# Kernel tuning notes

Measured on AMD Instinct MI355X. Metric: run time of the kernel, lower is better.

The kernel has to match this reference:

```python
import jax, jax.numpy as jnp
import numpy as np

N, E, G = 100000, 3200000, 5000
EPS = 1e-5
HEADS, HC = 8, 16


def setup_inputs() -> dict:
    key = jax.random.key(0)
    k = jax.random.split(key, 12)

    def lin(kk, fi, fo):
        return (jax.random.normal(kk, (fi, fo), jnp.float32) / np.sqrt(fi)).astype(jnp.float32)

    return {
        "x": jax.random.normal(k[0], (N, 20), jnp.float32),
        "edge_index": jax.random.randint(k[1], (2, E), 0, N, dtype=jnp.int32),
        "batch": jnp.sort(jax.random.randint(k[2], (N,), 0, G, dtype=jnp.int32)),
        "W1": lin(k[3], 20, 64), "b1": jnp.zeros((64,), jnp.float32),
        "g1": jnp.ones((64,), jnp.float32), "be1": jnp.zeros((64,), jnp.float32),
        "W2": lin(k[4], 64, 32), "b2": jnp.zeros((32,), jnp.float32),
        "g2": jnp.ones((32,), jnp.float32), "be2": jnp.zeros((32,), jnp.float32),
        "W3": lin(k[5], 32, 16), "b3": jnp.zeros((16,), jnp.float32),
        "g3": jnp.ones((16,), jnp.float32), "be3": jnp.zeros((16,), jnp.float32),
        "Wg": lin(k[6], 16, HEADS * HC),
        "att_src": jax.random.normal(k[7], (HEADS, HC), jnp.float32) * 0.1,
        "att_dst": jax.random.normal(k[8], (HEADS, HC), jnp.float32) * 0.1,
        "bg": jnp.zeros((HC,), jnp.float32),
        "Wf": lin(k[9], 16, 3), "bf": jnp.zeros((3,), jnp.float32),
    }


def reference(x, edge_index, batch,
              W1, b1, g1, be1, W2, b2, g2, be2, W3, b3, g3, be3,
              Wg, att_src, att_dst, bg, Wf, bf):
    src, dst = edge_index[0], edge_index[1]
    loop = jnp.arange(N, dtype=src.dtype)
    src_sl = jnp.concatenate([src, loop])  # self-loops (GCN + GAT add_self_loops)
    dst_sl = jnp.concatenate([dst, loop])

    # GCN symmetric normalization D^-1/2 (A+I) D^-1/2
    deg = jax.ops.segment_sum(jnp.ones_like(src_sl, dtype=jnp.float32), dst_sl, N)
    dinv = jnp.where(deg > 0, 1.0 / jnp.sqrt(deg), 0.0)
    norm = (dinv[src_sl] * dinv[dst_sl])[:, None]  # [E+N, 1]

    def gcn(h, W, b):
        h = h @ W
        return jax.ops.segment_sum(h[src_sl] * norm, dst_sl, N) + b

    def bn_relu(h, g, b):  # BatchNorm1d (train-mode batch stats) + ReLU
        mu = h.mean(0)
        var = ((h - mu) ** 2).mean(0)
        return jax.nn.relu(g * (h - mu) * jax.lax.rsqrt(var + EPS) + b)

    h = bn_relu(gcn(x, W1, b1), g1, be1)   # dropout = identity (eval)
    h = bn_relu(gcn(h, W2, b2), g2, be2)
    h = bn_relu(gcn(h, W3, b3), g3, be3)

    # GATConv: heads=8, concat=False (mean over heads), eval -> no dropout
    xg = (h @ Wg).reshape(N, HEADS, HC)
    a_src = (xg * att_src).sum(-1)  # [N, H]
    a_dst = (xg * att_dst).sum(-1)
    logit = jax.nn.leaky_relu(a_src[src_sl] + a_dst[dst_sl], 0.2)  # [E+N, H]
    m = jax.ops.segment_max(logit, dst_sl, N)          # segment softmax over dst
    e = jnp.exp(logit - m[dst_sl])
    s = jax.ops.segment_sum(e, dst_sl, N)
    alpha = e / s[dst_sl]
    agg = jax.ops.segment_sum(xg[src_sl] * alpha[:, :, None], dst_sl, N)  # [N,H,C]
    hg = agg.mean(1) + bg  # [N, 16]

    pooled = jax.ops.segment_sum(hg, batch, G)  # global_add_pool -> [G, 16]
    return pooled @ Wf + bf  # [G, 3]
```

## Files before the change

### kernel.cpp

```cpp
#include <hip/hip_runtime.h>
#include <hip/hip_fp16.h>

constexpr int NN = 100000;
constexpr int EE = 3200000;
constexpr int GG = 5000;
constexpr float BNEPS = 1e-5f;

constexpr int BINS = 128;
constexpr int NPB = (NN + BINS - 1) / BINS;
constexpr int BCHUNK = 8192;
constexpr int NBCH = (EE + BCHUNK - 1) / BCHUNK;
constexpr int BINCAP2 = 96;
constexpr int BINREG = 27648;
constexpr int LCAP = 26624;
constexpr int CTR_STRIDE = 32;

typedef int int4v __attribute__((ext_vector_type(4)));


__global__ __launch_bounds__(1024) void bin_edges(const int* __restrict__ ei,
                                                  uint2* __restrict__ pairs,
                                                  int* __restrict__ binCur) {
    __shared__ int bcnt[BINS];
    __shared__ int bbase[BINS];
    __shared__ uint2 buf[BINS][BINCAP2];
    const int t = threadIdx.x;
    const int lane = t & 63, wv = t >> 6;
    for (int ch = blockIdx.x; ch < NBCH; ch += gridDim.x) {
        for (int k = t; k < BINS; k += 1024) bcnt[k] = 0;
        __syncthreads();
        const int qbase = ch * (BCHUNK / 4);
#pragma unroll
        for (int rep = 0; rep < 2; ++rep) {
            const int q = qbase + rep * 1024 + t;
            if (q < EE / 4) {
                int4v d = __builtin_nontemporal_load((const int4v*)(ei + EE) + q);
                int4v s = __builtin_nontemporal_load((const int4v*)ei + q);
                int dd[4] = {d.x, d.y, d.z, d.w};
                int ss[4] = {s.x, s.y, s.z, s.w};
#pragma unroll
                for (int k = 0; k < 4; ++k) {
                    int o = dd[k] / NPB;
                    int p = atomicAdd(&bcnt[o], 1);
                    if (p < BINCAP2) {
                        buf[o][p] = make_uint2((unsigned)dd[k], (unsigned)ss[k]);
                    } else {
                        int gp = atomicAdd(&binCur[o * CTR_STRIDE], 1);
                        pairs[(size_t)o * BINREG + gp] =
                            make_uint2((unsigned)dd[k], (unsigned)ss[k]);
                    }
                }
            }
        }
        __syncthreads();
        if (t < BINS) {
            int c = bcnt[t] < BINCAP2 ? bcnt[t] : BINCAP2;
            bbase[t] = atomicAdd(&binCur[t * CTR_STRIDE], c);
            bcnt[t] = c;
        }
        __syncthreads();
        for (int o = wv; o < BINS; o += 16) {
            const int c = bcnt[o];
            const size_t base = (size_t)o * BINREG + bbase[o];
            for (int k = lane; k < c; k += 64) pairs[base + k] = buf[o][k];
        }
        __syncthreads();
    }
}


__global__ void bin_base(const int* __restrict__ binCur, int* __restrict__ binBase) {
    __shared__ int s[BINS];
    const int t = threadIdx.x;
    const int v = binCur[t * CTR_STRIDE];
    s[t] = v;
    __syncthreads();
    for (int off = 1; off < BINS; off <<= 1) {
        int add = (t >= off) ? s[t - off] : 0;
        __syncthreads();
        s[t] += add;
        __syncthreads();
    }
    binBase[t] = s[t] - v;
}


__global__ __launch_bounds__(1024) void scatter_lds(const uint2* __restrict__ pairs,
                                                    const int* __restrict__ binCur,
                                                    const int* __restrict__ binBase,
                                                    int* __restrict__ rowptr,
                                                    float* __restrict__ dinv,
                                                    int* __restrict__ colA) {
    __shared__ int scnt[NPB];
    __shared__ int sscan[1024];
    __shared__ int lbuf[LCAP];
    const int b = blockIdx.x;
    const int t = threadIdx.x;
    const int lo = b * NPB;
    const int hi = (lo + NPB < NN) ? lo + NPB : NN;
    const int nb = hi - lo;
    const int tot = binCur[b * CTR_STRIDE];
    const int base = binBase[b];
    const uint2* p = pairs + (size_t)b * BINREG;
    for (int k = t; k < nb; k += 1024) scnt[k] = 0;
    __syncthreads();
    for (int q = t; q < tot; q += 1024) atomicAdd(&scnt[p[q].x - lo], 1);
    __syncthreads();
    const int myc = (t < nb) ? scnt[t] : 0;
    sscan[t] = myc;
    __syncthreads();
    for (int off = 1; off < 1024; off <<= 1) {
        int add = (t >= off) ? sscan[t - off] : 0;
        __syncthreads();
        sscan[t] += add;
        __syncthreads();
    }
    const int excl = sscan[t] - myc;
    if (t < nb) {
        rowptr[lo + t] = base + excl;
        dinv[lo + t] = rsqrtf((float)(myc + 1));
        scnt[t] = excl;
    }
    if (b == BINS - 1 && t == 0) rowptr[NN] = base + tot;
    __syncthreads();
    for (int q = t; q < tot; q += 1024) {
        uint2 e = p[q];
        int pos = atomicAdd(&scnt[e.x - lo], 1);
        if (pos < LCAP) lbuf[pos] = (int)e.y;
        else colA[base + pos] = (int)e.y;
    }
    __syncthreads();
    const int m = tot < LCAP ? tot : LCAP;
    for (int k = t; k < m; k += 1024) colA[base + k] = lbuf[k];
}


__global__ void scale_x(const float* __restrict__ x, const float* __restrict__ dinv,
                        __half* __restrict__ xsc) {
    int idx = blockIdx.x * blockDim.x + threadIdx.x;
    if (idx < NN * 20) {
        int n = idx / 20;
        xsc[idx] = __float2half(x[idx] * dinv[n]);
    }
}


template <int FIN, int FOUT, bool AFFINE, bool SCALED, bool STATS>
__global__ void gemm_k(const float* __restrict__ hin,
                       const float* __restrict__ sumsIn, const float* __restrict__ ssqIn,
                       const float* __restrict__ g, const float* __restrict__ be,
                       const float* __restrict__ W, const float* __restrict__ dinv,
                       const float* __restrict__ bias,
                       float* __restrict__ outF, __half* __restrict__ outH,
                       float* __restrict__ sumsOut, float* __restrict__ ssqOut) {
    constexpr int NB = 256 / FOUT;
    __shared__ float Wl[FIN * FOUT];
    __shared__ float rows[NB][FIN];
    __shared__ float aa[AFFINE ? FIN : 1], bb[AFFINE ? FIN : 1];
    const int t = threadIdx.x;
    if constexpr (AFFINE) {
        if (t < FIN) {
            float mu = sumsIn[t] / (float)NN;
            float var = ssqIn[t] / (float)NN - mu * mu;
            float a = g[t] * rsqrtf(var + BNEPS);
            aa[t] = a;
            bb[t] = be[t] - mu * a;
        }
    }
    for (int i = t; i < FIN * FOUT; i += 256) Wl[i] = W[i];
    const int c = t % FOUT, s = t / FOUT;
    const int ngrp = (NN + NB - 1) / NB;
    float sAcc = 0.f, qAcc = 0.f;
    for (int grp = blockIdx.x; grp < ngrp; grp += gridDim.x) {
        __syncthreads();
        for (int i = t; i < NB * FIN; i += 256) {
            int sn = i / FIN, k = i % FIN;
            int n2 = grp * NB + sn;
            float v = 0.f;
            if (n2 < NN) {
                v = hin[(size_t)n2 * FIN + k];
                if constexpr (AFFINE) {
                    v = aa[k] * v + bb[k];
                    v = v > 0.f ? v : 0.f;
                }
            }
            rows[sn][k] = v;
        }
        __syncthreads();
        int node = grp * NB + s;
        if (node < NN) {
            float acc = 0.f;
#pragma unroll
            for (int k = 0; k < FIN; ++k) acc += rows[s][k] * Wl[k * FOUT + c];
            if constexpr (SCALED) {
                outH[(size_t)node * FOUT + c] = __float2half(acc * dinv[node]);
            } else {
                float val = acc + bias[c];
                outF[(size_t)node * FOUT + c] = val;
                if constexpr (STATS) { sAcc += val; qAcc += val * val; }
            }
        }
    }
    if constexpr (STATS) {
        __shared__ float ls[FOUT], lq[FOUT];
        __syncthreads();
        if (t < FOUT) { ls[t] = 0.f; lq[t] = 0.f; }
        __syncthreads();
        atomicAdd(&ls[c], sAcc);
        atomicAdd(&lq[c], qAcc);
        __syncthreads();
        if (t < FOUT) { atomicAdd(&sumsOut[t], ls[t]); atomicAdd(&ssqOut[t], lq[t]); }
    }
}


template <int H2, int OUTF, bool STATS>
__global__ void agg_half(const __half2* __restrict__ src, const int* __restrict__ rowptr,
                         const int* __restrict__ colA, const float* __restrict__ dinv,
                         const float* __restrict__ bias, float* __restrict__ out,
                         float* __restrict__ sumsOut, float* __restrict__ ssqOut) {
    constexpr int SUB = 64 / H2;
    const int lane = threadIdx.x & 63;
    const int wid = (blockIdx.x * blockDim.x + threadIdx.x) >> 6;
    const int totalWaves = (gridDim.x * blockDim.x) >> 6;
    const int f = lane % H2;
    const int sub = lane / H2;
    const int stride = totalWaves * SUB;
    float bx = 0.f, by = 0.f;
    if (bias != nullptr) {
        bx = bias[2 * f];
        by = (2 * f + 1 < OUTF) ? bias[2 * f + 1] : 0.f;
    }
    const int i0 = (sub < SUB) ? wid * SUB + sub : NN;
    float sx = 0.f, qx = 0.f, sy = 0.f, qy = 0.f;
    for (int i = i0; i < NN; i += stride) {
        const int r0 = rowptr[i], r1 = rowptr[i + 1];
        float2 acc = __half22float2(src[(size_t)i * H2 + f]);
        float2 acc2 = {0.f, 0.f};
        int e = r0;
        for (; e + 3 < r1; e += 4) {
            int j0 = colA[e], j1 = colA[e + 1], j2 = colA[e + 2], j3 = colA[e + 3];
            float2 v0 = __half22float2(src[(size_t)j0 * H2 + f]);
            float2 v1 = __half22float2(src[(size_t)j1 * H2 + f]);
            float2 v2 = __half22float2(src[(size_t)j2 * H2 + f]);
            float2 v3 = __half22float2(src[(size_t)j3 * H2 + f]);
            acc.x += v0.x + v1.x;
            acc.y += v0.y + v1.y;
            acc2.x += v2.x + v3.x;
            acc2.y += v2.y + v3.y;
        }
        for (; e < r1; ++e) {
            float2 v = __half22float2(src[(size_t)colA[e] * H2 + f]);
            acc.x += v.x; acc.y += v.y;
        }
        acc.x += acc2.x; acc.y += acc2.y;
        const float d = dinv[i];
        float vx = d * acc.x + bx;
        out[(size_t)i * OUTF + 2 * f] = vx;
        if constexpr (STATS) { sx += vx; qx += vx * vx; }
        if (2 * f + 1 < OUTF) {
            float vy = d * acc.y + by;
            out[(size_t)i * OUTF + 2 * f + 1] = vy;
            if constexpr (STATS) { sy += vy; qy += vy * vy; }
        }
    }
    if constexpr (STATS) {
        __shared__ float ls[OUTF], lq[OUTF];
        const int t = threadIdx.x;
        if (t < OUTF) { ls[t] = 0.f; lq[t] = 0.f; }
        __syncthreads();
        atomicAdd(&ls[2 * f], sx);
        atomicAdd(&lq[2 * f], qx);
        if (2 * f + 1 < OUTF) {
            atomicAdd(&ls[2 * f + 1], sy);
            atomicAdd(&lq[2 * f + 1], qy);
        }
        __syncthreads();
        if (t < OUTF) { atomicAdd(&sumsOut[t], ls[t]); atomicAdd(&ssqOut[t], lq[t]); }
    }
}


__global__ void gat_mats(const float* __restrict__ Wg, const float* __restrict__ att_src,
                         const float* __restrict__ att_dst, const float* __restrict__ Wf,
                         const float* __restrict__ bg, float* __restrict__ Psrc,
                         float* __restrict__ Pdst, float* __restrict__ M,
                         float* __restrict__ bgW) {
    int t = threadIdx.x;
    if (t < 128) {
        int k = t >> 3, h = t & 7;
        float s = 0.f, d = 0.f;
        for (int c = 0; c < 16; ++c) {
            float wv = Wg[k * 128 + h * 16 + c];
            s += wv * att_src[h * 16 + c];
            d += wv * att_dst[h * 16 + c];
        }
        Psrc[k * 8 + h] = s;
        Pdst[k * 8 + h] = d;
    } else if (t < 512) {
        int m = t - 128;
        if (m < 384) {
            int hk = m / 3, j = m - hk * 3;
            int H = hk >> 4, k = hk & 15;
            float s = 0.f;
            for (int c = 0; c < 16; ++c) s += Wg[k * 128 + H * 16 + c] * Wf[c * 3 + j];
            M[hk * 3 + j] = 0.125f * s;
        }
    } else if (t < 515) {
        int j = t - 512;
        float s = 0.f;
        for (int c = 0; c < 16; ++c) s += bg[c] * Wf[c * 3 + j];
        bgW[j] = s;
    }
}


__global__ void gat_pre2(const float* __restrict__ h3,
                         const float* __restrict__ sums3, const float* __restrict__ ssq3,
                         const float* __restrict__ g3, const float* __restrict__ be3,
                         const float* __restrict__ Psrc, const float* __restrict__ Pdst,
                         __half* __restrict__ z, float* __restrict__ asrc,
                         float* __restrict__ adst) {
    __shared__ float Ps[128], Pd[128], aa[16], bb[16];
    int t = threadIdx.x;
    if (t < 128) { Ps[t] = Psrc[t]; Pd[t] = Pdst[t]; }
    if (t < 16) {
        float mu = sums3[t] / (float)NN;
        float var = ssq3[t] / (float)NN - mu * mu;
        float a = g3[t] * rsqrtf(var + BNEPS);
        aa[t] = a;
        bb[t] = be3[t] - mu * a;
    }
    __syncthreads();
    int n = blockIdx.x * blockDim.x + t;
    if (n >= NN) return;
    float zv[16];
#pragma unroll
    for (int k = 0; k < 16; ++k) {
        float v = h3[(size_t)n * 16 + k];
        v = aa[k] * v + bb[k];
        zv[k] = v > 0.f ? v : 0.f;
    }
    __half2 zh[8];
#pragma unroll
    for (int k = 0; k < 8; ++k) zh[k] = __floats2half2_rn(zv[2 * k], zv[2 * k + 1]);
    float4* zo = (float4*)(z + (size_t)n * 16);
    zo[0] = ((float4*)zh)[0];
    zo[1] = ((float4*)zh)[1];
    float as[8], ad[8];
#pragma unroll
    for (int h = 0; h < 8; ++h) { as[h] = 0.f; ad[h] = 0.f; }
#pragma unroll
    for (int k = 0; k < 16; ++k) {
        float zk = zv[k];
#pragma unroll
        for (int h = 0; h < 8; ++h) {
            as[h] += zk * Ps[k * 8 + h];
            ad[h] += zk * Pd[k * 8 + h];
        }
    }
    float4* a4 = (float4*)(asrc + (size_t)n * 8);
    a4[0] = make_float4(as[0], as[1], as[2], as[3]);
    a4[1] = make_float4(as[4], as[5], as[6], as[7]);
    float4* d4 = (float4*)(adst + (size_t)n * 8);
    d4[0] = make_float4(ad[0], ad[1], ad[2], ad[3]);
    d4[1] = make_float4(ad[4], ad[5], ad[6], ad[7]);
}


__device__ __forceinline__ float leaky02(float x) { return x > 0.f ? x : 0.2f * x; }

__global__ void gat_agg5(const float2* __restrict__ z2, const float* __restrict__ asrc,
                         const float* __restrict__ adst, const int* __restrict__ rowptr,
                         const int* __restrict__ colA, __half* __restrict__ Sn) {
    const int lane = threadIdx.x & 63;
    const int q = lane & 3;
    const int hh = (lane >> 2) & 1;
    const int sub = lane >> 3;
    const int wid = (blockIdx.x * blockDim.x + threadIdx.x) >> 6;
    const int totalWaves = (gridDim.x * blockDim.x) >> 6;
    const float4* asrc4 = (const float4*)asrc;
    const float4* adst4 = (const float4*)adst;
    for (int i = wid; i < NN; i += totalWaves) {
        const int r0 = rowptr[i], r1 = rowptr[i + 1];
        const float4 adh = adst4[(size_t)i * 2 + hh];
        float acc[4][4];
        float wsum[4];
        {
            float4 a = asrc4[(size_t)i * 2 + hh];
            float2 zr = z2[(size_t)i * 4 + q];
            const __half2* zp = (const __half2*)&zr;
            float2 f0 = __half22float2(zp[0]), f1 = __half22float2(zp[1]);
            float zf[4] = {f0.x, f0.y, f1.x, f1.y};
            float wq[4];
            wq[0] = (sub == 0) ? __expf(leaky02(a.x + adh.x)) : 0.f;
            wq[1] = (sub == 0) ? __expf(leaky02(a.y + adh.y)) : 0.f;
            wq[2] = (sub == 0) ? __expf(leaky02(a.z + adh.z)) : 0.f;
            wq[3] = (sub == 0) ? __expf(leaky02(a.w + adh.w)) : 0.f;
#pragma unroll
            for (int h = 0; h < 4; ++h) {
                wsum[h] = wq[h];
#pragma unroll
                for (int k = 0; k < 4; ++k) acc[h][k] = wq[h] * zf[k];
            }
        }
        for (int e = r0; e < r1; e += 8) {
            const int ee = e + sub;
            const bool val = ee < r1;
            const int j = val ? colA[ee] : i;
            float4 a = asrc4[(size_t)j * 2 + hh];
            float2 zr = z2[(size_t)j * 4 + q];
            const __half2* zp = (const __half2*)&zr;
            float2 f0 = __half22float2(zp[0]), f1 = __half22float2(zp[1]);
            float zf[4] = {f0.x, f0.y, f1.x, f1.y};
            float wq[4];
            wq[0] = val ? __expf(leaky02(a.x + adh.x)) : 0.f;
            wq[1] = val ? __expf(leaky02(a.y + adh.y)) : 0.f;
            wq[2] = val ? __expf(leaky02(a.z + adh.z)) : 0.f;
            wq[3] = val ? __expf(leaky02(a.w + adh.w)) : 0.f;
#pragma unroll
            for (int h = 0; h < 4; ++h) {
                wsum[h] += wq[h];
#pragma unroll
                for (int k = 0; k < 4; ++k) acc[h][k] += wq[h] * zf[k];
            }
        }
#pragma unroll
        for (int off = 8; off < 64; off <<= 1) {
#pragma unroll
            for (int h = 0; h < 4; ++h) {
                wsum[h] += __shfl_xor(wsum[h], off);
#pragma unroll
                for (int k = 0; k < 4; ++k) acc[h][k] += __shfl_xor(acc[h][k], off);
            }
        }
        if (lane < 8) {
#pragma unroll
            for (int h = 0; h < 4; ++h) {
                const float inv = 1.f / wsum[h];
                __half2 o[2];
                o[0] = __floats2half2_rn(acc[h][0] * inv, acc[h][1] * inv);
                o[1] = __floats2half2_rn(acc[h][2] * inv, acc[h][3] * inv);
                *(float2*)(Sn + (size_t)i * 128 + (hh * 4 + h) * 16 + q * 4) = *(float2*)o;
            }
        }
    }
}


__global__ void graph_bounds(const int* __restrict__ batch, int* __restrict__ gstart) {
    int n = blockIdx.x * blockDim.x + threadIdx.x;
    if (n < NN) {
        int bn = batch[n];
        int bp = (n == 0) ? -1 : batch[n - 1];
        for (int g = bp + 1; g <= bn; ++g) gstart[g] = n;
        if (n == NN - 1)
            for (int g = bn + 1; g <= GG; ++g) gstart[g] = NN;
    }
}


__global__ void pool_final(const __half2* __restrict__ Sn2, const int* __restrict__ gstart,
                           const float* __restrict__ M, const float* __restrict__ bgW,
                           const float* __restrict__ bf, float* __restrict__ out) {
    const int lane = threadIdx.x & 63;
    const int g = (blockIdx.x * blockDim.x + threadIdx.x) >> 6;
    if (g >= GG) return;
    const int n0 = gstart[g], n1 = gstart[g + 1];
    float2 s = {0.f, 0.f};
    for (int n = n0; n < n1; ++n) {
        float2 v = __half22float2(Sn2[(size_t)n * 64 + lane]);
        s.x += v.x;
        s.y += v.y;
    }
    float o[3];
#pragma unroll
    for (int j = 0; j < 3; ++j)
        o[j] = s.x * M[(2 * lane) * 3 + j] + s.y * M[(2 * lane + 1) * 3 + j];
#pragma unroll
    for (int off = 1; off < 64; off <<= 1) {
#pragma unroll
        for (int j = 0; j < 3; ++j) o[j] += __shfl_xor(o[j], off);
    }
    if (lane == 0) {
        float cnt = (float)(n1 - n0);
#pragma unroll
        for (int j = 0; j < 3; ++j) out[g * 3 + j] = o[j] + cnt * bgW[j] + bf[j];
    }
}


extern "C" void kernel_launch(void* const* d_in, const int* in_sizes, int n_in,
                              void* d_out, int out_size, void* d_ws, size_t ws_size,
                              hipStream_t stream) {
    const float* x = (const float*)d_in[0];
    const int* ei = (const int*)d_in[1];
    const int* batch = (const int*)d_in[2];
    const float* W1 = (const float*)d_in[3];  const float* b1 = (const float*)d_in[4];
    const float* g1 = (const float*)d_in[5];  const float* be1 = (const float*)d_in[6];
    const float* W2 = (const float*)d_in[7];  const float* b2 = (const float*)d_in[8];
    const float* g2 = (const float*)d_in[9];  const float* be2 = (const float*)d_in[10];
    const float* W3 = (const float*)d_in[11]; const float* b3 = (const float*)d_in[12];
    const float* g3 = (const float*)d_in[13]; const float* be3 = (const float*)d_in[14];
    const float* Wg = (const float*)d_in[15];
    const float* att_src = (const float*)d_in[16];
    const float* att_dst = (const float*)d_in[17];
    const float* bg = (const float*)d_in[18];
    const float* Wf = (const float*)d_in[19];
    const float* bf = (const float*)d_in[20];
    float* out = (float*)d_out;

    char* w = (char*)d_ws;
    auto alloc = [&](size_t bytes) -> char* {
        char* p = w;
        w += (bytes + 255) & ~(size_t)255;
        return p;
    };
    int* binCur = (int*)alloc((size_t)BINS * CTR_STRIDE * 4);
    float* sums1 = (float*)alloc(64 * 4); float* ssq1 = (float*)alloc(64 * 4);
    float* sums2 = (float*)alloc(32 * 4); float* ssq2 = (float*)alloc(32 * 4);
    float* sums3 = (float*)alloc(16 * 4); float* ssq3 = (float*)alloc(16 * 4);
    size_t zeroBytes = (size_t)(w - (char*)d_ws);
    int* binBase = (int*)alloc((size_t)BINS * 4);
    float* Psrc = (float*)alloc(128 * 4);
    float* Pdst = (float*)alloc(128 * 4);
    float* Mm = (float*)alloc(384 * 4);
    float* bgW = (float*)alloc(3 * 4);
    int* gstart = (int*)alloc((size_t)(GG + 1) * 4);
    int* rowptr = (int*)alloc((size_t)(NN + 1) * 4);
    int* colA = (int*)alloc((size_t)EE * 4);
    float* dinv = (float*)alloc((size_t)NN * 4);
    char* A = alloc((size_t)NN * 64 * 4);
    char* B = alloc((size_t)NN * 64 * 4);

    uint2*  pairs = (uint2*)A;
    __half* xsc  = (__half*)B;
    float*  aggx = (float*)(B + (size_t)NN * 32 * 2);
    float*  h1   = (float*)A;
    __half* hs2  = (__half*)B;
    float*  h2   = (float*)(B + (size_t)NN * 32 * 2);
    __half* hs3  = (__half*)A;
    float*  h3   = (float*)(A + (size_t)NN * 16 * 2);
    __half* z    = (__half*)(A + (size_t)NN * 24 * 4);
    float*  asrc = (float*)(A + (size_t)NN * 32 * 4);
    float*  adst = (float*)(A + (size_t)NN * 40 * 4);
    __half* Sn   = (__half*)B;

    hipMemsetAsync(d_ws, 0, zeroBytes, stream);

    bin_edges<<<256, 1024, 0, stream>>>(ei, pairs, binCur);
    bin_base<<<1, BINS, 0, stream>>>(binCur, binBase);
    scatter_lds<<<BINS, 1024, 0, stream>>>(pairs, binCur, binBase, rowptr, dinv, colA);
    gat_mats<<<1, 1024, 0, stream>>>(Wg, att_src, att_dst, Wf, bg, Psrc, Pdst, Mm, bgW);
    graph_bounds<<<(NN + 255) / 256, 256, 0, stream>>>(batch, gstart);

    scale_x<<<(NN * 20 + 255) / 256, 256, 0, stream>>>(x, dinv, xsc);
    agg_half<10, 20, false><<<2048, 256, 0, stream>>>((const __half2*)xsc, rowptr, colA, dinv,
                                                      nullptr, aggx, nullptr, nullptr);
    gemm_k<20, 64, false, false, true><<<2048, 256, 0, stream>>>(
        aggx, nullptr, nullptr, nullptr, nullptr, W1, dinv, b1, h1, nullptr, sums1, ssq1);

    gemm_k<64, 32, true, true, false><<<2048, 256, 0, stream>>>(
        h1, sums1, ssq1, g1, be1, W2, dinv, nullptr, nullptr, hs2, nullptr, nullptr);
    agg_half<16, 32, true><<<2048, 256, 0, stream>>>((const __half2*)hs2, rowptr, colA, dinv,
                                                     b2, h2, sums2, ssq2);

    gemm_k<32, 16, true, true, false><<<2048, 256, 0, stream>>>(
        h2, sums2, ssq2, g2, be2, W3, dinv, nullptr, nullptr, hs3, nullptr, nullptr);
    agg_half<8, 16, true><<<2048, 256, 0, stream>>>((const __half2*)hs3, rowptr, colA, dinv,
                                                    b3, h3, sums3, ssq3);

    gat_pre2<<<(NN + 255) / 256, 256, 0, stream>>>(h3, sums3, ssq3, g3, be3, Psrc, Pdst,
                                                   z, asrc, adst);
    gat_agg5<<<2048, 256, 0, stream>>>((const float2*)z, asrc, adst, rowptr, colA, Sn);
    pool_final<<<(GG * 64 + 255) / 256, 256, 0, stream>>>((const __half2*)Sn, gstart, Mm, bgW,
                                                          bf, out);
}
```

Baseline: 516.4 us.

## Pack GAT source logits with features in half-precision rows, unroll edge loop

Stores the per-node attention source logits as fp16 next to the fp16 node features in one 64-byte row, so each gathered neighbour needs a single cache line instead of two separate arrays. The GAT aggregation loop is unrolled to process two edges per sub-lane per iteration for more loads in flight. Edge-index loads in the GCN and GAT aggregations use nontemporal hints to avoid polluting cache. Rounding the source logits to fp16 adds precision risk in the softmax.

```diff
diff --git a/kernel.cpp b/kernel.cpp
--- a/kernel.cpp
+++ b/kernel.cpp
@@ -239,7 +239,10 @@
         float2 acc2 = {0.f, 0.f};
         int e = r0;
         for (; e + 3 < r1; e += 4) {
-            int j0 = colA[e], j1 = colA[e + 1], j2 = colA[e + 2], j3 = colA[e + 3];
+            int j0 = __builtin_nontemporal_load(&colA[e]);
+            int j1 = __builtin_nontemporal_load(&colA[e + 1]);
+            int j2 = __builtin_nontemporal_load(&colA[e + 2]);
+            int j3 = __builtin_nontemporal_load(&colA[e + 3]);
             float2 v0 = __half22float2(src[(size_t)j0 * H2 + f]);
             float2 v1 = __half22float2(src[(size_t)j1 * H2 + f]);
             float2 v2 = __half22float2(src[(size_t)j2 * H2 + f]);
@@ -250,7 +253,7 @@
             acc2.y += v2.y + v3.y;
         }
         for (; e < r1; ++e) {
-            float2 v = __half22float2(src[(size_t)colA[e] * H2 + f]);
+            float2 v = __half22float2(src[(size_t)__builtin_nontemporal_load(&colA[e]) * H2 + f]);
             acc.x += v.x; acc.y += v.y;
         }
         acc.x += acc2.x; acc.y += acc2.y;
@@ -315,12 +318,11 @@
 }
 
 
-__global__ void gat_pre2(const float* __restrict__ h3,
+__global__ void gat_pre3(const float* __restrict__ h3,
                          const float* __restrict__ sums3, const float* __restrict__ ssq3,
                          const float* __restrict__ g3, const float* __restrict__ be3,
                          const float* __restrict__ Psrc, const float* __restrict__ Pdst,
-                         __half* __restrict__ z, float* __restrict__ asrc,
-                         float* __restrict__ adst) {
+                         __half* __restrict__ zc, float* __restrict__ adst) {
     __shared__ float Ps[128], Pd[128], aa[16], bb[16];
     int t = threadIdx.x;
     if (t < 128) { Ps[t] = Psrc[t]; Pd[t] = Pdst[t]; }
@@ -341,12 +343,6 @@
         v = aa[k] * v + bb[k];
         zv[k] = v > 0.f ? v : 0.f;
     }
-    __half2 zh[8];
-#pragma unroll
-    for (int k = 0; k < 8; ++k) zh[k] = __floats2half2_rn(zv[2 * k], zv[2 * k + 1]);
-    float4* zo = (float4*)(z + (size_t)n * 16);
-    zo[0] = ((float4*)zh)[0];
-    zo[1] = ((float4*)zh)[1];
     float as[8], ad[8];
 #pragma unroll
     for (int h = 0; h < 8; ++h) { as[h] = 0.f; ad[h] = 0.f; }
@@ -359,9 +355,16 @@
             ad[h] += zk * Pd[k * 8 + h];
         }
     }
-    float4* a4 = (float4*)(asrc + (size_t)n * 8);
-    a4[0] = make_float4(as[0], as[1], as[2], as[3]);
-    a4[1] = make_float4(as[4], as[5], as[6], as[7]);
+    __half2 ah[4];
+#pragma unroll
+    for (int k = 0; k < 4; ++k) ah[k] = __floats2half2_rn(as[2 * k], as[2 * k + 1]);
+    __half2 zh[8];
+#pragma unroll
+    for (int k = 0; k < 8; ++k) zh[k] = __floats2half2_rn(zv[2 * k], zv[2 * k + 1]);
+    __half* row = zc + (size_t)n * 32;
+    *(float4*)(row) = *(float4*)ah;
+    *(float4*)(row + 8) = ((float4*)zh)[0];
+    *(float4*)(row + 16) = ((float4*)zh)[1];
     float4* d4 = (float4*)(adst + (size_t)n * 8);
     d4[0] = make_float4(ad[0], ad[1], ad[2], ad[3]);
     d4[1] = make_float4(ad[4], ad[5], ad[6], ad[7]);
@@ -370,33 +373,37 @@
 
 __device__ __forceinline__ float leaky02(float x) { return x > 0.f ? x : 0.2f * x; }
 
-__global__ void gat_agg5(const float2* __restrict__ z2, const float* __restrict__ asrc,
-                         const float* __restrict__ adst, const int* __restrict__ rowptr,
-                         const int* __restrict__ colA, __half* __restrict__ Sn) {
+__global__ void gat_agg6(const __half* __restrict__ zc, const float* __restrict__ adst,
+                         const int* __restrict__ rowptr, const int* __restrict__ colA,
+                         __half* __restrict__ Sn) {
     const int lane = threadIdx.x & 63;
     const int q = lane & 3;
     const int hh = (lane >> 2) & 1;
     const int sub = lane >> 3;
     const int wid = (blockIdx.x * blockDim.x + threadIdx.x) >> 6;
     const int totalWaves = (gridDim.x * blockDim.x) >> 6;
-    const float4* asrc4 = (const float4*)asrc;
     const float4* adst4 = (const float4*)adst;
+    const int aoff = hh * 4;
+    const int zoff = 8 + q * 4;
     for (int i = wid; i < NN; i += totalWaves) {
         const int r0 = rowptr[i], r1 = rowptr[i + 1];
         const float4 adh = adst4[(size_t)i * 2 + hh];
         float acc[4][4];
         float wsum[4];
         {
-            float4 a = asrc4[(size_t)i * 2 + hh];
-            float2 zr = z2[(size_t)i * 4 + q];
-            const __half2* zp = (const __half2*)&zr;
+            const __half* row = zc + (size_t)i * 32;
+            float2 araw = *(const float2*)(row + aoff);
+            const __half2* ah = (const __half2*)&araw;
+            float2 a01 = __half22float2(ah[0]), a23 = __half22float2(ah[1]);
+            float2 zraw = *(const float2*)(row + zoff);
+            const __half2* zp = (const __half2*)&zraw;
             float2 f0 = __half22float2(zp[0]), f1 = __half22float2(zp[1]);
             float zf[4] = {f0.x, f0.y, f1.x, f1.y};
             float wq[4];
-            wq[0] = (sub == 0) ? __expf(leaky02(a.x + adh.x)) : 0.f;
-            wq[1] = (sub == 0) ? __expf(leaky02(a.y + adh.y)) : 0.f;
-            wq[2] = (sub == 0) ? __expf(leaky02(a.z + adh.z)) : 0.f;
-            wq[3] = (sub == 0) ? __expf(leaky02(a.w + adh.w)) : 0.f;
+            wq[0] = (sub == 0) ? __expf(leaky02(a01.x + adh.x)) : 0.f;
+            wq[1] = (sub == 0) ? __expf(leaky02(a01.y + adh.y)) : 0.f;
+            wq[2] = (sub == 0) ? __expf(leaky02(a23.x + adh.z)) : 0.f;
+            wq[3] = (sub == 0) ? __expf(leaky02(a23.y + adh.w)) : 0.f;
 #pragma unroll
             for (int h = 0; h < 4; ++h) {
                 wsum[h] = wq[h];
@@ -404,25 +411,52 @@
                 for (int k = 0; k < 4; ++k) acc[h][k] = wq[h] * zf[k];
             }
         }
-        for (int e = r0; e < r1; e += 8) {
-            const int ee = e + sub;
-            const bool val = ee < r1;
-            const int j = val ? colA[ee] : i;
-            float4 a = asrc4[(size_t)j * 2 + hh];
-            float2 zr = z2[(size_t)j * 4 + q];
-            const __half2* zp = (const __half2*)&zr;
-            float2 f0 = __half22float2(zp[0]), f1 = __half22float2(zp[1]);
-            float zf[4] = {f0.x, f0.y, f1.x, f1.y};
-            float wq[4];
-            wq[0] = val ? __expf(leaky02(a.x + adh.x)) : 0.f;
-            wq[1] = val ? __expf(leaky02(a.y + adh.y)) : 0.f;
-            wq[2] = val ? __expf(leaky02(a.z + adh.z)) : 0.f;
-            wq[3] = val ? __expf(leaky02(a.w + adh.w)) : 0.f;
-#pragma unroll
-            for (int h = 0; h < 4; ++h) {
-                wsum[h] += wq[h];
-#pragma unroll
-                for (int k = 0; k < 4; ++k) acc[h][k] += wq[h] * zf[k];
+        for (int e = r0; e < r1; e += 16) {
+            const int ee0 = e + sub, ee1 = e + 8 + sub;
+            const bool v0 = ee0 < r1, v1 = ee1 < r1;
+            const int j0 = v0 ? __builtin_nontemporal_load(&colA[ee0]) : i;
+            const int j1 = v1 ? __builtin_nontemporal_load(&colA[ee1]) : i;
+            const __half* row0 = zc + (size_t)j0 * 32;
+            const __half* row1 = zc + (size_t)j1 * 32;
+            float2 araw0 = *(const float2*)(row0 + aoff);
+            float2 zraw0 = *(const float2*)(row0 + zoff);
+            float2 araw1 = *(const float2*)(row1 + aoff);
+            float2 zraw1 = *(const float2*)(row1 + zoff);
+            {
+                const __half2* ah = (const __half2*)&araw0;
+                float2 a01 = __half22float2(ah[0]), a23 = __half22float2(ah[1]);
+                const __half2* zp = (const __half2*)&zraw0;
+                float2 f0 = __half22float2(zp[0]), f1 = __half22float2(zp[1]);
+                float zf[4] = {f0.x, f0.y, f1.x, f1.y};
+                float wq[4];
+                wq[0] = v0 ? __expf(leaky02(a01.x + adh.x)) : 0.f;
+                wq[1] = v0 ? __expf(leaky02(a01.y + adh.y)) : 0.f;
+                wq[2] = v0 ? __expf(leaky02(a23.x + adh.z)) : 0.f;
+                wq[3] = v0 ? __expf(leaky02(a23.y + adh.w)) : 0.f;
+#pragma unroll
+                for (int h = 0; h < 4; ++h) {
+                    wsum[h] += wq[h];
+#pragma unroll
+                    for (int k = 0; k < 4; ++k) acc[h][k] += wq[h] * zf[k];
+                }
+            }
+            {
+                const __half2* ah = (const __half2*)&araw1;
+                float2 a01 = __half22float2(ah[0]), a23 = __half22float2(ah[1]);
+                const __half2* zp = (const __half2*)&zraw1;
+                float2 f0 = __half22float2(zp[0]), f1 = __half22float2(zp[1]);
+                float zf[4] = {f0.x, f0.y, f1.x, f1.y};
+                float wq[4];
+                wq[0] = v1 ? __expf(leaky02(a01.x + adh.x)) : 0.f;
+                wq[1] = v1 ? __expf(leaky02(a01.y + adh.y)) : 0.f;
+                wq[2] = v1 ? __expf(leaky02(a23.x + adh.z)) : 0.f;
+                wq[3] = v1 ? __expf(leaky02(a23.y + adh.w)) : 0.f;
+#pragma unroll
+                for (int h = 0; h < 4; ++h) {
+                    wsum[h] += wq[h];
+#pragma unroll
+                    for (int k = 0; k < 4; ++k) acc[h][k] += wq[h] * zf[k];
+                }
             }
         }
 #pragma unroll
@@ -541,8 +575,7 @@
     float*  h2   = (float*)(B + (size_t)NN * 32 * 2);
     __half* hs3  = (__half*)A;
     float*  h3   = (float*)(A + (size_t)NN * 16 * 2);
-    __half* z    = (__half*)(A + (size_t)NN * 24 * 4);
-    float*  asrc = (float*)(A + (size_t)NN * 32 * 4);
+    __half* zc   = (__half*)(A + (size_t)NN * 24 * 4);
     float*  adst = (float*)(A + (size_t)NN * 40 * 4);
     __half* Sn   = (__half*)B;
 
@@ -570,9 +603,9 @@
     agg_half<8, 16, true><<<2048, 256, 0, stream>>>((const __half2*)hs3, rowptr, colA, dinv,
                                                     b3, h3, sums3, ssq3);
 
-    gat_pre2<<<(NN + 255) / 256, 256, 0, stream>>>(h3, sums3, ssq3, g3, be3, Psrc, Pdst,
-                                                   z, asrc, adst);
-    gat_agg5<<<2048, 256, 0, stream>>>((const float2*)z, asrc, adst, rowptr, colA, Sn);
+    gat_pre3<<<(NN + 255) / 256, 256, 0, stream>>>(h3, sums3, ssq3, g3, be3, Psrc, Pdst,
+                                                   zc, adst);
+    gat_agg6<<<2048, 256, 0, stream>>>(zc, adst, rowptr, colA, Sn);
     pool_final<<<(GG * 64 + 255) / 256, 256, 0, stream>>>((const __half2*)Sn, gstart, Mm, bgW,
                                                           bf, out);
 }
```

After: 556.0 us. 7.7% more time.
